# Kernel optimization log

Measured on AMD Instinct MI355X. Metric: run time of the kernel, lower is better.

Reference implementation:

```python
import jax, jax.numpy as jnp
import numpy as np
import math

C_S = 384; C_Z = 128; C_H = 16; H = 12; PQ = 4; PV = 8; C_SURF = 16
N_RES = 512; N_SURF = 2048; B = 1
INF = 1e5; EPS = 1e-8
SOFTPLUS_INV_1 = 0.541324854612918


def _quat_to_rot(q):
    q = q / jnp.linalg.norm(q, axis=-1, keepdims=True)
    w, x, y, z = q[..., 0], q[..., 1], q[..., 2], q[..., 3]
    R = jnp.stack([
        1 - 2 * (y * y + z * z), 2 * (x * y - w * z), 2 * (x * z + w * y),
        2 * (x * y + w * z), 1 - 2 * (x * x + z * z), 2 * (y * z - w * x),
        2 * (x * z - w * y), 2 * (y * z + w * x), 1 - 2 * (x * x + y * y),
    ], axis=-1)
    return R.reshape(q.shape[:-1] + (3, 3))


def setup_inputs() -> dict:
    key = jax.random.key(0)
    ks = jax.random.split(key, 32)
    hc = H * C_H            # 192
    hpq = H * PQ * 3        # 144
    hpkv = H * (PQ + PV) * 3  # 432
    cz4 = C_Z // 4
    concat = hc + H * PV * 3 + H * PV + H * cz4 + hc  # 1152
    w = lambda k, i, o: jax.random.normal(k, (i, o), jnp.float32) * 0.02
    inp = {
        's': jax.random.normal(ks[0], (B, N_RES, C_S), jnp.float32),
        'z': jax.random.normal(ks[1], (B, N_RES, N_RES, C_Z), jnp.float32),
        'rots': _quat_to_rot(jax.random.normal(ks[2], (B, N_RES, 4), jnp.float32)),
        'trans': jax.random.normal(ks[3], (B, N_RES, 3), jnp.float32) * 10.0,
        'mask': jnp.ones((B, N_RES), jnp.float32),
        'surface_points': jax.random.normal(ks[4], (B, N_SURF, 3), jnp.float32) * 10.0,
        'surface_features': jax.random.normal(ks[5], (B, N_SURF, C_SURF), jnp.float32),
        'surface_mask': jnp.ones((B, N_SURF), jnp.float32),
        'Wq': w(ks[6], C_S, hc), 'bq': jnp.zeros((hc,)),
        'Wkv': w(ks[7], C_S, 2 * hc), 'bkv': jnp.zeros((2 * hc,)),
        'Wqp': w(ks[8], C_S, hpq), 'bqp': jnp.zeros((hpq,)),
        'Wkvp': w(ks[9], C_S, hpkv), 'bkvp': jnp.zeros((hpkv,)),
        'Wse': w(ks[10], C_SURF, C_S), 'bse': jnp.zeros((C_S,)),
        'Wsq': w(ks[11], C_S, hc), 'bsq': jnp.zeros((hc,)),
        'Wsk': w(ks[12], C_S, hc), 'bsk': jnp.zeros((hc,)),
        'Wsv': w(ks[13], C_S, hc), 'bsv': jnp.zeros((hc,)),
        'Wb': w(ks[14], C_Z, H), 'bb': jnp.zeros((H,)),
        'Wdz': w(ks[15], C_Z, cz4), 'bdz': jnp.zeros((cz4,)),
        'head_weights': jnp.full((H,), SOFTPLUS_INV_1, jnp.float32),
        'sb_weights': jnp.full((1,), SOFTPLUS_INV_1, jnp.float32),
        'Wout': w(ks[16], concat, C_S), 'bout': jnp.zeros((C_S,)),
        'Wso': w(ks[17], 2 * C_S, C_SURF), 'bso': jnp.zeros((C_SURF,)),
    }
    return inp


def reference(s, z, rots, trans, mask, surface_points, surface_features, surface_mask,
              Wq, bq, Wkv, bkv, Wqp, bqp, Wkvp, bkvp, Wse, bse, Wsq, bsq, Wsk, bsk,
              Wsv, bsv, Wb, bb, Wdz, bdz, head_weights, sb_weights, Wout, bout, Wso, bso):
    lin = lambda x, W, b: x @ W + b
    b_, n, _ = s.shape
    m = surface_points.shape[-2]

    surface_feat = lin(surface_features, Wse, bse)                    # [B,M,c_s]
    # backbone<->surface squared distances
    disp = trans[:, :, None, :] - surface_points[:, None, :, :]       # [B,N,M,3]
    dist_sq = jnp.sum(disp * disp, -1)                                # [B,N,M]

    q = lin(s, Wq, bq).reshape(b_, n, H, C_H)
    kv = lin(s, Wkv, bkv).reshape(b_, n, H, 2 * C_H)
    k, v = kv[..., :C_H], kv[..., C_H:]

    # query points: split into 3 coord chunks, stack, rigid-apply
    qp = lin(s, Wqp, bqp)
    qp = jnp.stack(jnp.split(qp, 3, axis=-1), axis=-1)                # [B,N,H*PQ,3]
    qp = jnp.einsum('bnij,bnpj->bnpi', rots, qp) + trans[:, :, None]
    qp = qp.reshape(b_, n, H, PQ, 3)

    kvp = lin(s, Wkvp, bkvp)
    kvp = jnp.stack(jnp.split(kvp, 3, axis=-1), axis=-1)              # [B,N,H*(PQ+PV),3]
    kvp = jnp.einsum('bnij,bnpj->bnpi', rots, kvp) + trans[:, :, None]
    kvp = kvp.reshape(b_, n, H, PQ + PV, 3)
    kp, vp = kvp[..., :PQ, :], kvp[..., PQ:, :]

    b_bias = lin(z, Wb, bb)                                           # [B,N,N,H]
    a = jnp.einsum('bihc,bjhc->bhij', q, k) * math.sqrt(1.0 / (3 * C_H))
    a = a + math.sqrt(1.0 / 3) * jnp.transpose(b_bias, (0, 3, 1, 2))

    # point-distance attention term
    pt = jnp.sum((qp[:, :, None] - kp[:, None]) ** 2, axis=-1)        # [B,N,N,H,PQ]
    hw = jax.nn.softplus(head_weights)                                # [H]
    pt = jnp.sum(pt, axis=-1) * hw * math.sqrt(1.0 / (3 * (PQ * 9.0 / 2))) * (-0.5)
    a = a + jnp.transpose(pt, (0, 3, 1, 2))                           # [B,H,N,N]

    sq_mask = INF * (mask[:, :, None] * mask[:, None, :] - 1.0)
    a = jax.nn.softmax(a + sq_mask[:, None], axis=-1)

    o = jnp.einsum('bhij,bjhc->bihc', a, v).reshape(b_, n, H * C_H)
    o_pt = jnp.einsum('bhij,bjhpd->bihpd', a, vp)                     # [B,N,H,PV,3]
    o_pt = jnp.einsum('bnji,bnhpj->bnhpi', rots, o_pt - trans[:, :, None, None])
    o_pt_norm = jnp.sqrt(jnp.sum(o_pt ** 2, -1) + EPS).reshape(b_, n, H * PV)
    o_pt_flat = o_pt.reshape(b_, n, H * PV, 3)

    pair_z = lin(z, Wdz, bdz)                                         # [B,N,N,cz/4]
    o_pair = jnp.einsum('bhij,bijc->bihc', a, pair_z).reshape(b_, n, -1)

    # surface cross-attention branch
    sq = lin(s, Wsq, bsq).reshape(b_, n, H, C_H)
    sk = lin(surface_feat, Wsk, bsk).reshape(b_, m, H, C_H)
    sv = lin(surface_feat, Wsv, bsv).reshape(b_, m, H, C_H)
    logits = jnp.einsum('bnhc,bmhc->bhnm', sq, sk) * math.sqrt(1.0 / C_H)
    sbw = jax.nn.softplus(sb_weights)[0]
    logits = logits - 0.5 * sbw * dist_sq[:, None]
    cross_mask = mask[:, :, None] * surface_mask[:, None, :]          # [B,N,M]
    logits = logits + INF * (cross_mask - 1.0)[:, None]
    a_s = jax.nn.softmax(logits, axis=-1)
    o_surf = jnp.einsum('bhnm,bmhc->bnhc', a_s, sv).reshape(b_, n, H * C_H)

    o_cat = jnp.concatenate([o, o_pt_flat[..., 0], o_pt_flat[..., 1], o_pt_flat[..., 2],
                             o_pt_norm, o_pair, o_surf], axis=-1)
    s_out = lin(o_cat, Wout, bout)                                    # [B,N,c_s]

    # surface update: attend surface points to backbone (softmax over residues)
    a_ts = jax.nn.softmax(jnp.swapaxes(logits, -1, -2), axis=-1).mean(axis=1)  # [B,M,N]
    s_agg = jnp.einsum('bmn,bnc->bmc', a_ts, s)
    surf_out = lin(jnp.concatenate([surface_feat, s_agg], axis=-1), Wso, bso)
    return s_out, surf_out
```

## Files before the change

### kernel.cpp

```cpp
#include <hip/hip_runtime.h>
#include <cstddef>


#define CS 384
#define INFV 100000.0f

__device__ __forceinline__ float softplusf(float x) { return log1pf(__expf(x)); }

__global__ __launch_bounds__(256) void k_pack(
    const float* __restrict__ Wq, const float* __restrict__ Wsq,
    const float* __restrict__ Wkv, const float* __restrict__ Wqp,
    const float* __restrict__ Wkvp, const float* __restrict__ Wsk,
    const float* __restrict__ Wsv, const float* __restrict__ Wout,
    const float* __restrict__ bq, const float* __restrict__ bsq,
    const float* __restrict__ bkv, const float* __restrict__ bqp,
    const float* __restrict__ bkvp, const float* __restrict__ bsk,
    const float* __restrict__ bsv,
    float* __restrict__ wt1, float* __restrict__ wt2, float* __restrict__ wt3,
    float* __restrict__ b1, float* __restrict__ b2)
{
    const int b = blockIdx.x, t = threadIdx.x;
    if (b >= 1092) {
        int idx = (b - 1092) * 256 + t;
        if (idx < 1344) {
            float v;
            if (idx < 192) v = bq[idx];
            else if (idx < 384) v = bsq[idx - 192];
            else if (idx < 768) v = bkv[idx - 384];
            else if (idx < 912) v = bqp[idx - 768];
            else v = bkvp[idx - 912];
            b1[idx] = v;
        } else if (idx < 1728) {
            int i2 = idx - 1344;
            b2[i2] = (i2 < 192) ? bsk[i2] : bsv[i2 - 192];
        }
        return;
    }
    const float* src; float* dst; int C, coff, tile, ldd;
    if (b < 72)       { src = Wq;   C = 192; dst = wt1; coff = 0;   ldd = 384;  tile = b; }
    else if (b < 144) { src = Wsq;  C = 192; dst = wt1; coff = 192; ldd = 384;  tile = b - 72; }
    else if (b < 288) { src = Wkv;  C = 384; dst = wt1; coff = 384; ldd = 384;  tile = b - 144; }
    else if (b < 348) { src = Wqp;  C = 144; dst = wt1; coff = 768; ldd = 384;  tile = b - 288; }
    else if (b < 516) { src = Wkvp; C = 432; dst = wt1; coff = 912; ldd = 384;  tile = b - 348; }
    else if (b < 588) { src = Wsk;  C = 192; dst = wt2; coff = 0;   ldd = 384;  tile = b - 516; }
    else if (b < 660) { src = Wsv;  C = 192; dst = wt2; coff = 192; ldd = 384;  tile = b - 588; }
    else              { src = Wout; C = 384; dst = wt3; coff = 0;   ldd = 1152; tile = b - 660; }
    const int cT = (C + 31) >> 5;
    const int tk = tile / cT, tc = tile % cT;
    __shared__ float l[32][33];
    const int tr = t >> 5, tcc = t & 31;
    #pragma unroll
    for (int rr = 0; rr < 4; ++rr) {
        int kloc = tr * 4 + rr;
        int cg = tc * 32 + tcc;
        l[kloc][tcc] = (cg < C) ? src[(size_t)(tk * 32 + kloc) * C + cg] : 0.f;
    }
    __syncthreads();
    #pragma unroll
    for (int rr = 0; rr < 4; ++rr) {
        int cloc = tr * 4 + rr;
        int cg = tc * 32 + cloc;
        if (cg < C) dst[(size_t)(coff + cg) * ldd + tk * 32 + tcc] = l[tcc][cloc];
    }
}

__global__ __launch_bounds__(256) void k_packz(
    const float* __restrict__ Wb, const float* __restrict__ bb,
    const float* __restrict__ Wdz, const float* __restrict__ bdz,
    float* __restrict__ wz, float* __restrict__ bz)
{
    const float s3 = 0.5773502691896258f;
    int idx = blockIdx.x * 256 + threadIdx.x;
    if (idx < 5632) {
        int c = idx >> 7, kk = idx & 127;
        wz[idx] = (c < 12) ? s3 * Wb[kk * 12 + c] : Wdz[kk * 32 + (c - 12)];
    } else if (idx < 5676) {
        int c = idx - 5632;
        bz[c] = (c < 12) ? s3 * bb[c] : bdz[c - 12];
    }
}

__global__ __launch_bounds__(256) void k_transp(
    const float* __restrict__ A, float* __restrict__ At)
{
    __shared__ float tile[32][33];
    const int r0 = blockIdx.y * 32, c0 = blockIdx.x * 32;
    const int tr = threadIdx.x >> 5, tc = threadIdx.x & 31;
    #pragma unroll
    for (int rr = 0; rr < 4; ++rr)
        tile[tr + rr * 8][tc] = A[(size_t)(r0 + tr + rr * 8) * 384 + c0 + tc];
    __syncthreads();
    #pragma unroll
    for (int rr = 0; rr < 4; ++rr)
        At[(size_t)(c0 + tr + rr * 8) * 512 + r0 + tc] = tile[tc][tr + rr * 8];
}

template<int KTOT, bool HB>
__global__ __launch_bounds__(256) void k_gemm(
    const float* __restrict__ A, const float* __restrict__ Wt,
    const float* __restrict__ bias, float* __restrict__ C, int ldc)
{
    __shared__ float As[64][68];
    __shared__ float Ws[64][68];
    const int t = threadIdx.x;
    const int c0 = blockIdx.x * 64, m0 = blockIdx.y * 64;
    const int sr = t >> 4, sk4 = (t & 15) << 2;
    const int wid = t >> 6, lane = t & 63;
    const int wr = (wid >> 1) * 32, wc = (wid & 1) * 32;
    const int lr = lane >> 3, lc = lane & 7;
    float acc[4][4];
    #pragma unroll
    for (int j = 0; j < 4; ++j) {
        float bv = HB ? bias[c0 + wc + lc + 8 * j] : 0.f;
        #pragma unroll
        for (int i = 0; i < 4; ++i) acc[i][j] = bv;
    }
    for (int kc = 0; kc < KTOT; kc += 64) {
        __syncthreads();
        #pragma unroll
        for (int rep = 0; rep < 4; ++rep) {
            int row = sr + rep * 16;
            *(float4*)&As[row][sk4] = *(const float4*)&A[(size_t)(m0 + row) * KTOT + kc + sk4];
            *(float4*)&Ws[row][sk4] = *(const float4*)&Wt[(size_t)(c0 + row) * KTOT + kc + sk4];
        }
        __syncthreads();
        #pragma unroll 4
        for (int k4 = 0; k4 < 16; ++k4) {
            float4 a[4], w[4];
            #pragma unroll
            for (int i = 0; i < 4; ++i) a[i] = *(float4*)&As[wr + lr + 8 * i][k4 * 4];
            #pragma unroll
            for (int j = 0; j < 4; ++j) w[j] = *(float4*)&Ws[wc + lc + 8 * j][k4 * 4];
            #pragma unroll
            for (int i = 0; i < 4; ++i) {
                #pragma unroll
                for (int j = 0; j < 4; ++j) {
                    acc[i][j] = fmaf(a[i].x, w[j].x, acc[i][j]);
                    acc[i][j] = fmaf(a[i].y, w[j].y, acc[i][j]);
                    acc[i][j] = fmaf(a[i].z, w[j].z, acc[i][j]);
                    acc[i][j] = fmaf(a[i].w, w[j].w, acc[i][j]);
                }
            }
        }
    }
    #pragma unroll
    for (int i = 0; i < 4; ++i) {
        #pragma unroll
        for (int j = 0; j < 4; ++j)
            C[(size_t)(m0 + wr + lr + 8 * i) * ldc + c0 + wc + lc + 8 * j] = acc[i][j];
    }
}

__global__ __launch_bounds__(256) void k_scatter(
    const float* __restrict__ proj, const float* __restrict__ rots,
    const float* __restrict__ trans,
    float* __restrict__ qw, float* __restrict__ kw, float* __restrict__ vw,
    float* __restrict__ sqw, float* __restrict__ qpw, float* __restrict__ kpw,
    float* __restrict__ vpw)
{
    __shared__ float p[4][1344];
    const int n0 = blockIdx.x * 4, t = threadIdx.x;
    for (int idx = t; idx < 1344; idx += 256) {
        #pragma unroll
        for (int r = 0; r < 4; ++r) p[r][idx] = proj[(size_t)(n0 + r) * 1344 + idx];
    }
    __syncthreads();
    for (int idx = t; idx < 3072; idx += 256) {
        int r = idx / 768, c = idx % 768;
        int n = n0 + r;
        float v = p[r][c];
        if (c < 192) qw[(size_t)n * 192 + c] = v;
        else if (c < 384) sqw[(size_t)n * 192 + (c - 192)] = v;
        else {
            int cc = c - 384, h = cc >> 5, sub = cc & 31;
            if (sub < 16) kw[(size_t)n * 192 + h * 16 + sub] = v;
            else          vw[(size_t)n * 192 + h * 16 + (sub - 16)] = v;
        }
    }
    for (int idx = t; idx < 2304; idx += 256) {
        int r = idx / 576, rem = idx % 576;
        int n = n0 + r;
        const float* R = &rots[(size_t)n * 9];
        const float* tr = &trans[(size_t)n * 3];
        if (rem < 144) {
            int pp = rem / 3, d = rem % 3;
            float v = fmaf(R[d*3+0], p[r][768 + pp],
                      fmaf(R[d*3+1], p[r][768 + 48 + pp],
                      fmaf(R[d*3+2], p[r][768 + 96 + pp], tr[d])));
            qpw[(size_t)n * 144 + pp * 3 + d] = v;
        } else {
            int rem2 = rem - 144; int pp = rem2 / 3, d = rem2 % 3;
            float v = fmaf(R[d*3+0], p[r][912 + pp],
                      fmaf(R[d*3+1], p[r][912 + 144 + pp],
                      fmaf(R[d*3+2], p[r][912 + 288 + pp], tr[d])));
            int h = pp / 12, ii = pp % 12;
            if (ii < 4) kpw[(size_t)n * 144 + h * 12 + ii * 3 + d] = v;
            else        vpw[(size_t)n * 288 + h * 24 + (ii - 4) * 3 + d] = v;
        }
    }
}

__global__ __launch_bounds__(256) void k_sfeat(
    const float* __restrict__ sf, const float* __restrict__ Wse,
    const float* __restrict__ bse, float* __restrict__ sfeat)
{
    __shared__ float wl[16 * 384];
    __shared__ float sfl[8][16];
    const int m0 = blockIdx.x * 8, t = threadIdx.x;
    for (int idx = t; idx < 6144; idx += 256) wl[idx] = Wse[idx];
    if (t < 128) sfl[t >> 4][t & 15] = sf[(size_t)(m0 + (t >> 4)) * 16 + (t & 15)];
    __syncthreads();
    #pragma unroll
    for (int u = 0; u < 12; ++u) {
        int idx = t + u * 256;
        int r = idx / 384, c = idx % 384;
        float a = bse[c];
        #pragma unroll
        for (int kk = 0; kk < 16; ++kk) a = fmaf(sfl[r][kk], wl[kk * 384 + c], a);
        sfeat[(size_t)(m0 + r) * 384 + c] = a;
    }
}

__global__ __launch_bounds__(256) void k_zpass(
    const float* __restrict__ z, const float* __restrict__ wz,
    const float* __restrict__ bz, float* __restrict__ bpz)
{
    __shared__ float zt[64][132];
    const int i = blockIdx.x, t = threadIdx.x;
    const int jbase = blockIdx.y * 256;
    const int jl = t & 63;
    const int cgs = __builtin_amdgcn_readfirstlane(t >> 6);
    const float* __restrict__ wp = wz + cgs * 11 * 128;
    float bv[11];
    #pragma unroll
    for (int u = 0; u < 11; ++u) bv[u] = bz[cgs * 11 + u];
    for (int ch = 0; ch < 4; ++ch) {
        const int j0 = jbase + ch * 64;
        __syncthreads();
        for (int idx = t; idx < 2048; idx += 256) {
            int r = idx >> 5, c4 = (idx & 31) << 2;
            *(float4*)&zt[r][c4] = *(const float4*)&z[((size_t)i * 512 + j0 + r) * 128 + c4];
        }
        __syncthreads();
        float acc[11];
        #pragma unroll
        for (int u = 0; u < 11; ++u) acc[u] = bv[u];
        #pragma unroll 2
        for (int k4 = 0; k4 < 128; k4 += 4) {
            float4 zv = *(float4*)&zt[jl][k4];
            #pragma unroll
            for (int u = 0; u < 11; ++u) {
                const float* w = wp + u * 128 + k4;
                acc[u] = fmaf(zv.x, w[0],
                         fmaf(zv.y, w[1],
                         fmaf(zv.z, w[2],
                         fmaf(zv.w, w[3], acc[u]))));
            }
        }
        #pragma unroll
        for (int u = 0; u < 11; ++u)
            bpz[((size_t)i * 44 + cgs * 11 + u) * 512 + j0 + jl] = acc[u];
    }
}

__global__ __launch_bounds__(256) void k_attn_a(
    const float* __restrict__ qw, const float* __restrict__ kw,
    const float* __restrict__ qpw, const float* __restrict__ kpw,
    const float* __restrict__ bpz, const float* __restrict__ mask,
    const float* __restrict__ hwp, float* __restrict__ abuf)
{
    __shared__ float pls[4][520];
    __shared__ float qs[64], qps[48], cpt4[4];
    const int i = blockIdx.x, hg = blockIdx.y;
    const int t = threadIdx.x;
    if (t < 64) qs[t] = qw[(size_t)i * 192 + hg * 64 + t];
    if (t < 48) qps[t] = qpw[(size_t)i * 144 + hg * 48 + t];
    if (t < 4) cpt4[t] = -0.5f * 0.13608276348795434f * softplusf(hwp[hg * 4 + t]);
    const float mask_i = mask[i];
    __syncthreads();
    #pragma unroll 2
    for (int it = 0; it < 8; ++it) {
        int idx = t + it * 256;
        int hh = idx >> 9, j = idx & 511;
        int h = hg * 4 + hh;
        float kj[16], kpj[12];
        { const float4* kr = (const float4*)&kw[(size_t)j * 192 + h * 16];
          *(float4*)&kj[0] = kr[0]; *(float4*)&kj[4] = kr[1];
          *(float4*)&kj[8] = kr[2]; *(float4*)&kj[12] = kr[3]; }
        { const float4* kr = (const float4*)&kpw[(size_t)j * 144 + h * 12];
          *(float4*)&kpj[0] = kr[0]; *(float4*)&kpj[4] = kr[1]; *(float4*)&kpj[8] = kr[2]; }
        float qk = 0.f;
        #pragma unroll
        for (int c = 0; c < 16; ++c) qk = fmaf(qs[hh * 16 + c], kj[c], qk);
        float pts = 0.f;
        #pragma unroll
        for (int p = 0; p < 4; ++p) {
            float dx = qps[hh*12+p*3+0] - kpj[p*3+0];
            float dy = qps[hh*12+p*3+1] - kpj[p*3+1];
            float dz = qps[hh*12+p*3+2] - kpj[p*3+2];
            pts += dx*dx + dy*dy + dz*dz;
        }
        float lg = fmaf(0.14433756729740643f, qk, bpz[((size_t)i * 44 + h) * 512 + j]);
        lg = fmaf(cpt4[hh], pts, lg);
        lg += INFV * (mask_i * mask[j] - 1.0f);
        pls[hh][j] = lg;
    }
    __syncthreads();
    const int w = t >> 6, lane = t & 63;
    float v[8];
    #pragma unroll
    for (int k = 0; k < 8; ++k) v[k] = pls[w][lane + k * 64];
    float mx = v[0];
    #pragma unroll
    for (int k = 1; k < 8; ++k) mx = fmaxf(mx, v[k]);
    #pragma unroll
    for (int off = 32; off; off >>= 1) mx = fmaxf(mx, __shfl_xor(mx, off));
    float sm = 0.f;
    #pragma unroll
    for (int k = 0; k < 8; ++k) { v[k] = __expf(v[k] - mx); sm += v[k]; }
    #pragma unroll
    for (int off = 32; off; off >>= 1) sm += __shfl_xor(sm, off);
    const float inv = 1.0f / sm;
    float* dst = abuf + ((size_t)(hg * 4 + w) * 512 + i) * 512;
    #pragma unroll
    for (int k = 0; k < 8; ++k) dst[lane + k * 64] = v[k] * inv;
}

__global__ __launch_bounds__(256) void k_attn_pair(
    const float* __restrict__ abuf, const float* __restrict__ bpz,
    float* __restrict__ ocat)
{
    __shared__ float al[12][512];
    const int i = blockIdx.x, t = threadIdx.x;
    #pragma unroll
    for (int u = 0; u < 12; ++u) {
        al[u][t] = abuf[(size_t)u * 262144 + (size_t)i * 512 + t];
        al[u][t + 256] = abuf[(size_t)u * 262144 + (size_t)i * 512 + t + 256];
    }
    __syncthreads();
    const int c = t & 31;
    const int h1 = t >> 5;
    const bool dual = (t < 128);
    const float* pz = bpz + ((size_t)i * 44 + 12 + c) * 512;
    const float* a1 = al[h1];
    const float* a2 = al[dual ? h1 + 8 : 0];
    float acc1 = 0.f, acc2 = 0.f;
    for (int j = 0; j < 512; j += 4) {
        float4 p = *(const float4*)&pz[j];
        acc1 = fmaf(a1[j+0], p.x, acc1);
        acc1 = fmaf(a1[j+1], p.y, acc1);
        acc1 = fmaf(a1[j+2], p.z, acc1);
        acc1 = fmaf(a1[j+3], p.w, acc1);
        if (dual) {
            acc2 = fmaf(a2[j+0], p.x, acc2);
            acc2 = fmaf(a2[j+1], p.y, acc2);
            acc2 = fmaf(a2[j+2], p.z, acc2);
            acc2 = fmaf(a2[j+3], p.w, acc2);
        }
    }
    ocat[(size_t)i * 1152 + 576 + h1 * 32 + c] = acc1;
    if (dual) ocat[(size_t)i * 1152 + 576 + (h1 + 8) * 32 + c] = acc2;
}

__global__ __launch_bounds__(256) void k_gemm_ov(
    const float* __restrict__ abuf, const float* __restrict__ vw,
    const float* __restrict__ vpw, float* __restrict__ cbuf)
{
    __shared__ float As[64][68];
    __shared__ float Bs[64][44];
    const int i0 = blockIdx.x * 64, h = blockIdx.y;
    const int t = threadIdx.x;
    const int sr = t >> 4, sk4 = (t & 15) << 2;
    const int r1 = t >> 3;
    const int cb = t & 7;
    float acc[2][5];
    #pragma unroll
    for (int u = 0; u < 5; ++u) { acc[0][u] = 0.f; acc[1][u] = 0.f; }
    for (int kc = 0; kc < 512; kc += 64) {
        __syncthreads();
        #pragma unroll
        for (int rep = 0; rep < 4; ++rep) {
            int row = sr + rep * 16;
            *(float4*)&As[row][sk4] =
                *(const float4*)&abuf[(size_t)h * 262144 + (size_t)(i0 + row) * 512 + kc + sk4];
        }
        #pragma unroll
        for (int u = 0; u < 10; ++u) {
            int idx = t + u * 256;
            int r = idx / 40, cc = idx % 40;
            Bs[r][cc] = (cc < 16) ? vw[(size_t)(kc + r) * 192 + h * 16 + cc]
                                  : vpw[(size_t)(kc + r) * 288 + h * 24 + (cc - 16)];
        }
        __syncthreads();
        #pragma unroll 4
        for (int kk = 0; kk < 64; ++kk) {
            float av1 = As[r1][kk], av2 = As[r1 + 32][kk];
            #pragma unroll
            for (int u = 0; u < 5; ++u) {
                float b = Bs[kk][cb + 8 * u];
                acc[0][u] = fmaf(av1, b, acc[0][u]);
                acc[1][u] = fmaf(av2, b, acc[1][u]);
            }
        }
    }
    #pragma unroll
    for (int u = 0; u < 5; ++u) {
        cbuf[((size_t)h * 512 + i0 + r1) * 40 + cb + 8 * u] = acc[0][u];
        cbuf[((size_t)h * 512 + i0 + r1 + 32) * 40 + cb + 8 * u] = acc[1][u];
    }
}

__global__ __launch_bounds__(256) void k_optfin(
    const float* __restrict__ cbuf, const float* __restrict__ rots,
    const float* __restrict__ trans, float* __restrict__ ocat)
{
    __shared__ float cl[4][12][40];
    const int i0 = blockIdx.x * 4, t = threadIdx.x;
    for (int idx = t; idx < 1920; idx += 256) {
        int ii = idx / 480, rem = idx % 480;
        int h = rem / 40, c = rem % 40;
        cl[ii][h][c] = cbuf[((size_t)h * 512 + i0 + ii) * 40 + c];
    }
    __syncthreads();
    for (int idx = t; idx < 768; idx += 256) {
        int ii = idx / 192, o = idx % 192;
        ocat[(size_t)(i0 + ii) * 1152 + o] = cl[ii][o >> 4][o & 15];
    }
    for (int idx = t; idx < 384; idx += 256) {
        int ii = idx / 96, hp = idx % 96;
        int h = hp >> 3, p = hp & 7;
        int i = i0 + ii;
        const float* R = &rots[(size_t)i * 9];
        float gx = cl[ii][h][16 + p*3 + 0] - trans[(size_t)i*3 + 0];
        float gy = cl[ii][h][16 + p*3 + 1] - trans[(size_t)i*3 + 1];
        float gz = cl[ii][h][16 + p*3 + 2] - trans[(size_t)i*3 + 2];
        float lx = R[0]*gx + R[3]*gy + R[6]*gz;
        float ly = R[1]*gx + R[4]*gy + R[7]*gz;
        float lz = R[2]*gx + R[5]*gy + R[8]*gz;
        float nm = sqrtf(lx*lx + ly*ly + lz*lz + 1e-8f);
        int col = h * 8 + p;
        size_t base = (size_t)i * 1152;
        ocat[base + 192 + col] = lx;
        ocat[base + 288 + col] = ly;
        ocat[base + 384 + col] = lz;
        ocat[base + 480 + col] = nm;
    }
}

__global__ __launch_bounds__(256) void k_surf(
    const float* __restrict__ sqw, const float* __restrict__ skv,
    const float* __restrict__ trans, const float* __restrict__ mask,
    const float* __restrict__ sp, const float* __restrict__ smask,
    const float* __restrict__ sbwp, float* __restrict__ ocat)
{
    __shared__ float sk_t[256][17];
    __shared__ float sv_t[256][17];
    __shared__ float sp_t[768];
    __shared__ float smask_t[256];
    const int h = blockIdx.x >> 5;
    const int n0 = (blockIdx.x & 31) * 16;
    const int t = threadIdx.x;
    const int tn = t >> 4, tm = t & 15;
    const int n = n0 + tn;
    const float sbw = softplusf(sbwp[0]);
    float qreg[16];
    #pragma unroll
    for (int c = 0; c < 16; ++c) qreg[c] = sqw[(size_t)n * 192 + h * 16 + c];
    const float trx = trans[(size_t)n*3+0], tryy = trans[(size_t)n*3+1], trz = trans[(size_t)n*3+2];
    const float mask_n = mask[n];
    float mx = -1e30f, l = 0.f;
    float acc[16];
    #pragma unroll
    for (int c = 0; c < 16; ++c) acc[c] = 0.f;
    for (int tile = 0; tile < 8; ++tile) {
        __syncthreads();
        const int mb = tile * 256;
        for (int idx = t; idx < 1024; idx += 256) {
            int ml = idx >> 2, c4 = (idx & 3) << 2;
            float4 v4 = *(const float4*)&skv[(size_t)(mb + ml) * 384 + h * 16 + c4];
            sk_t[ml][c4+0]=v4.x; sk_t[ml][c4+1]=v4.y; sk_t[ml][c4+2]=v4.z; sk_t[ml][c4+3]=v4.w;
            float4 w4 = *(const float4*)&skv[(size_t)(mb + ml) * 384 + 192 + h * 16 + c4];
            sv_t[ml][c4+0]=w4.x; sv_t[ml][c4+1]=w4.y; sv_t[ml][c4+2]=w4.z; sv_t[ml][c4+3]=w4.w;
        }
        for (int idx = t; idx < 768; idx += 256) sp_t[idx] = sp[(size_t)mb * 3 + idx];
        smask_t[t] = smask[mb + t];
        __syncthreads();
        float lgr[16];
        float tmax = -1e30f;
        #pragma unroll
        for (int kk = 0; kk < 16; ++kk) {
            int ml = tm + (kk << 4);
            float dot = 0.f;
            #pragma unroll
            for (int c = 0; c < 16; ++c) dot = fmaf(qreg[c], sk_t[ml][c], dot);
            float dx = trx - sp_t[ml*3+0], dy = tryy - sp_t[ml*3+1], dz = trz - sp_t[ml*3+2];
            float lg = fmaf(0.25f, dot, -0.5f * sbw * (dx*dx + dy*dy + dz*dz));
            lg += INFV * (mask_n * smask_t[ml] - 1.0f);
            lgr[kk] = lg;
            tmax = fmaxf(tmax, lg);
        }
        float mn = fmaxf(mx, tmax);
        float scale = __expf(mx - mn);
        l *= scale;
        #pragma unroll
        for (int c = 0; c < 16; ++c) acc[c] *= scale;
        #pragma unroll
        for (int kk = 0; kk < 16; ++kk) {
            int ml = tm + (kk << 4);
            float w = __expf(lgr[kk] - mn);
            l += w;
            #pragma unroll
            for (int c = 0; c < 16; ++c) acc[c] = fmaf(w, sv_t[ml][c], acc[c]);
        }
        mx = mn;
    }
    #pragma unroll
    for (int off = 1; off < 16; off <<= 1) {
        float m2 = __shfl_xor(mx, off), l2 = __shfl_xor(l, off);
        float mn = fmaxf(mx, m2);
        float e1 = __expf(mx - mn), e2 = __expf(m2 - mn);
        l = l * e1 + l2 * e2;
        #pragma unroll
        for (int c = 0; c < 16; ++c) {
            float a2 = __shfl_xor(acc[c], off);
            acc[c] = acc[c] * e1 + a2 * e2;
        }
        mx = mn;
    }
    const float invl = 1.0f / l;
    float outv = 0.f;
    #pragma unroll
    for (int c = 0; c < 16; ++c) if (tm == c) outv = acc[c];
    ocat[(size_t)n * 1152 + 960 + h * 16 + tm] = outv * invl;
}

__global__ __launch_bounds__(256) void k_tlog(
    const float* __restrict__ sqw, const float* __restrict__ skv,
    const float* __restrict__ trans, const float* __restrict__ mask,
    const float* __restrict__ sp, const float* __restrict__ smask,
    const float* __restrict__ sbwp, float* __restrict__ logits,
    float* __restrict__ stat_m, float* __restrict__ stat_il)
{
    __shared__ float sk_s[32][16];
    __shared__ float sq_s[32][16];
    __shared__ float trans_s[96];
    __shared__ float mask_s[32];
    __shared__ float spm_s[96];
    __shared__ float smask_s[32];
    const int h = blockIdx.y;
    const int m0 = blockIdx.x * 32;
    const int t = threadIdx.x;
    const int tmg = t >> 5, tnl = t & 31;
    const float sbw = softplusf(sbwp[0]);
    for (int idx = t; idx < 512; idx += 256) {
        int row = idx >> 4, c = idx & 15;
        sk_s[row][c] = skv[(size_t)(m0 + row) * 384 + h * 16 + c];
    }
    if (t < 96) spm_s[t] = sp[(size_t)m0 * 3 + t];
    if (t < 32) smask_s[t] = smask[m0 + t];
    __syncthreads();
    float skr[4][16];
    float spx[4], spy[4], spz[4], smk[4];
    #pragma unroll
    for (int mi = 0; mi < 4; ++mi) {
        int row = tmg * 4 + mi;
        #pragma unroll
        for (int c4 = 0; c4 < 16; c4 += 4)
            *(float4*)&skr[mi][c4] = *(float4*)&sk_s[row][c4];
        spx[mi] = spm_s[row*3+0]; spy[mi] = spm_s[row*3+1]; spz[mi] = spm_s[row*3+2];
        smk[mi] = smask_s[row];
    }
    float mxr[4], lr[4];
    #pragma unroll
    for (int mi = 0; mi < 4; ++mi) { mxr[mi] = -1e30f; lr[mi] = 0.f; }
    for (int nt = 0; nt < 16; ++nt) {
        __syncthreads();
        const int nb = nt * 32;
        if (t < 128) {
            int nn = t >> 2, c4 = (t & 3) << 2;
            *(float4*)&sq_s[nn][c4] = *(const float4*)&sqw[(size_t)(nb + nn) * 192 + h * 16 + c4];
        }
        if (t < 96) trans_s[t] = trans[(size_t)nb * 3 + t];
        if (t < 32) mask_s[t] = mask[nb + t];
        __syncthreads();
        float q[16];
        #pragma unroll
        for (int c4 = 0; c4 < 16; c4 += 4)
            *(float4*)&q[c4] = *(float4*)&sq_s[tnl][c4];
        const float tx = trans_s[tnl*3+0], ty = trans_s[tnl*3+1], tz = trans_s[tnl*3+2];
        const float mkn = mask_s[tnl];
        #pragma unroll
        for (int mi = 0; mi < 4; ++mi) {
            float dot = 0.f;
            #pragma unroll
            for (int c = 0; c < 16; ++c) dot = fmaf(skr[mi][c], q[c], dot);
            float dx = tx - spx[mi], dy = ty - spy[mi], dz = tz - spz[mi];
            float mterm = INFV * (mkn * smk[mi] - 1.0f) - 0.5f * sbw * (dx*dx + dy*dy + dz*dz);
            float lg = fmaf(0.25f, dot, mterm);
            logits[((size_t)(m0 + tmg * 4 + mi) * 12 + h) * 512 + nb + tnl] = lg;
            float newm = fmaxf(mxr[mi], lg);
            lr[mi] = lr[mi] * __expf(mxr[mi] - newm) + __expf(lg - newm);
            mxr[mi] = newm;
        }
    }
    #pragma unroll
    for (int off = 1; off < 32; off <<= 1) {
        #pragma unroll
        for (int mi = 0; mi < 4; ++mi) {
            float m2 = __shfl_xor(mxr[mi], off), l2 = __shfl_xor(lr[mi], off);
            float newm = fmaxf(mxr[mi], m2);
            lr[mi] = lr[mi] * __expf(mxr[mi] - newm) + l2 * __expf(m2 - newm);
            mxr[mi] = newm;
        }
    }
    if (tnl == 0) {
        #pragma unroll
        for (int mi = 0; mi < 4; ++mi) {
            int m = m0 + tmg * 4 + mi;
            stat_m[(size_t)m * 12 + h] = mxr[mi];
            stat_il[(size_t)m * 12 + h] = 1.0f / lr[mi];
        }
    }
}

__global__ __launch_bounds__(256) void k_tw(
    const float* __restrict__ logits, const float* __restrict__ stat_m,
    const float* __restrict__ stat_il, float* __restrict__ w)
{
    __shared__ float mxs[12], ils[12];
    const int m = blockIdx.x, t = threadIdx.x;
    if (t < 12) { mxs[t] = stat_m[(size_t)m * 12 + t]; ils[t] = stat_il[(size_t)m * 12 + t]; }
    __syncthreads();
    const float* lp = logits + (size_t)m * 12 * 512;
    float a0 = 0.f, a1 = 0.f;
    #pragma unroll
    for (int h = 0; h < 12; ++h) {
        a0 += __expf(lp[h * 512 + t] - mxs[h]) * ils[h];
        a1 += __expf(lp[h * 512 + 256 + t] - mxs[h]) * ils[h];
    }
    w[(size_t)m * 512 + t] = a0 * (1.0f / 12.0f);
    w[(size_t)m * 512 + 256 + t] = a1 * (1.0f / 12.0f);
}

__global__ __launch_bounds__(256) void k_surf_out(
    const float* __restrict__ sfeat, const float* __restrict__ saggw,
    const float* __restrict__ Wso, const float* __restrict__ bso,
    float* __restrict__ out)
{
    __shared__ float wl[12304];
    const int t = threadIdx.x;
    for (int idx = t; idx < 12288; idx += 256) {
        int k = idx >> 4, c = idx & 15;
        wl[(k / 192) * 3076 + (k % 192) * 16 + c] = Wso[idx];
    }
    const int m = blockIdx.x * 64 + (t >> 2);
    const int kq = t & 3;
    const float* src = (kq < 2) ? &sfeat[(size_t)m * 384 + kq * 192]
                                : &saggw[(size_t)m * 384 + (kq - 2) * 192];
    __syncthreads();
    float acc[16];
    #pragma unroll
    for (int c = 0; c < 16; ++c) acc[c] = 0.f;
    const float* wb = &wl[kq * 3076];
    for (int k = 0; k < 192; k += 4) {
        float4 v = *(const float4*)&src[k];
        #pragma unroll
        for (int e = 0; e < 4; ++e) {
            float sv = (&v.x)[e];
            #pragma unroll
            for (int c = 0; c < 16; ++c)
                acc[c] = fmaf(sv, wb[(k + e) * 16 + c], acc[c]);
        }
    }
    #pragma unroll
    for (int c = 0; c < 16; ++c) {
        acc[c] += __shfl_xor(acc[c], 1);
        acc[c] += __shfl_xor(acc[c], 2);
    }
    #pragma unroll
    for (int c = 0; c < 16; ++c) {
        if ((c >> 2) == kq) out[196608 + (size_t)m * 16 + c] = acc[c] + bso[c];
    }
}

extern "C" void kernel_launch(void* const* d_in, const int* in_sizes, int n_in,
                              void* d_out, int out_size, void* d_ws, size_t ws_size,
                              hipStream_t stream)
{
    (void)in_sizes; (void)n_in; (void)out_size; (void)ws_size;
    const float* s     = (const float*)d_in[0];
    const float* z     = (const float*)d_in[1];
    const float* rots  = (const float*)d_in[2];
    const float* trans = (const float*)d_in[3];
    const float* mask  = (const float*)d_in[4];
    const float* sp    = (const float*)d_in[5];
    const float* sf    = (const float*)d_in[6];
    const float* smask = (const float*)d_in[7];
    const float* Wq    = (const float*)d_in[8];  const float* bq   = (const float*)d_in[9];
    const float* Wkv   = (const float*)d_in[10]; const float* bkv  = (const float*)d_in[11];
    const float* Wqp   = (const float*)d_in[12]; const float* bqp  = (const float*)d_in[13];
    const float* Wkvp  = (const float*)d_in[14]; const float* bkvp = (const float*)d_in[15];
    const float* Wse   = (const float*)d_in[16]; const float* bse  = (const float*)d_in[17];
    const float* Wsq   = (const float*)d_in[18]; const float* bsq  = (const float*)d_in[19];
    const float* Wsk   = (const float*)d_in[20]; const float* bsk  = (const float*)d_in[21];
    const float* Wsv   = (const float*)d_in[22]; const float* bsv  = (const float*)d_in[23];
    const float* Wb    = (const float*)d_in[24]; const float* bb   = (const float*)d_in[25];
    const float* Wdz   = (const float*)d_in[26]; const float* bdz  = (const float*)d_in[27];
    const float* hw    = (const float*)d_in[28]; const float* sbw  = (const float*)d_in[29];
    const float* Wout  = (const float*)d_in[30]; const float* bout = (const float*)d_in[31];
    const float* Wso   = (const float*)d_in[32]; const float* bso  = (const float*)d_in[33];
    float* out = (float*)d_out;

    float* qw    = (float*)d_ws;
    float* kw    = qw    + (size_t)512 * 192;
    float* vw    = kw    + (size_t)512 * 192;
    float* sqw   = vw    + (size_t)512 * 192;
    float* qpw   = sqw   + (size_t)512 * 192;
    float* kpw   = qpw   + (size_t)512 * 144;
    float* vpw   = kpw   + (size_t)512 * 144;
    float* sfeat = vpw   + (size_t)512 * 288;
    float* skv   = sfeat + (size_t)2048 * 384;
    float* ocat  = skv   + (size_t)2048 * 384;
    float* sagg  = ocat  + (size_t)512 * 1152;
    float* region = sagg + (size_t)2048 * 384;
    float* proj   = region;
    float* bpz    = region;
    float* logits = region;
    float* wt1   = region + (size_t)2048 * 12 * 512;
    float* wt2   = wt1   + (size_t)1344 * 384;
    float* wt3   = wt2   + (size_t)384 * 384;
    float* b1    = wt3   + (size_t)384 * 1152;
    float* b2    = b1    + 1344;
    float* st    = b2    + 384;
    float* wbuf  = st    + (size_t)384 * 512;
    float* statm = wbuf  + (size_t)2048 * 512;
    float* stati = statm + (size_t)2048 * 12;
    float* abuf  = stati + (size_t)2048 * 12;
    float* cbuf  = abuf  + (size_t)12 * 512 * 512;
    float* wz    = cbuf  + (size_t)12 * 512 * 40;
    float* bz    = wz    + (size_t)44 * 128;

    k_pack<<<dim3(1099), dim3(256), 0, stream>>>(Wq, Wsq, Wkv, Wqp, Wkvp, Wsk, Wsv, Wout,
        bq, bsq, bkv, bqp, bkvp, bsk, bsv, wt1, wt2, wt3, b1, b2);
    k_packz<<<dim3(23), dim3(256), 0, stream>>>(Wb, bb, Wdz, bdz, wz, bz);
    k_transp<<<dim3(12, 16), dim3(256), 0, stream>>>(s, st);
    k_gemm<384, true><<<dim3(21, 8), dim3(256), 0, stream>>>(s, wt1, b1, proj, 1344);
    k_scatter<<<dim3(128), dim3(256), 0, stream>>>(proj, rots, trans,
        qw, kw, vw, sqw, qpw, kpw, vpw);
    k_sfeat<<<dim3(256), dim3(256), 0, stream>>>(sf, Wse, bse, sfeat);
    k_gemm<384, true><<<dim3(6, 32), dim3(256), 0, stream>>>(sfeat, wt2, b2, skv, 384);
    k_zpass<<<dim3(512, 2), dim3(256), 0, stream>>>(z, wz, bz, bpz);
    k_attn_a<<<dim3(512, 3), dim3(256), 0, stream>>>(qw, kw, qpw, kpw, bpz, mask, hw, abuf);
    k_attn_pair<<<dim3(512), dim3(256), 0, stream>>>(abuf, bpz, ocat);
    k_gemm_ov<<<dim3(8, 12), dim3(256), 0, stream>>>(abuf, vw, vpw, cbuf);
    k_optfin<<<dim3(128), dim3(256), 0, stream>>>(cbuf, rots, trans, ocat);
    k_surf<<<dim3(384), dim3(256), 0, stream>>>(sqw, skv, trans, mask, sp, smask,
        sbw, ocat);
    k_tlog<<<dim3(64, 12), dim3(256), 0, stream>>>(sqw, skv, trans, mask, sp, smask,
        sbw, logits, statm, stati);
    k_tw<<<dim3(2048), dim3(256), 0, stream>>>(logits, statm, stati, wbuf);
    k_gemm<512, false><<<dim3(6, 32), dim3(256), 0, stream>>>(wbuf, st, nullptr, sagg, 384);
    k_surf_out<<<dim3(32), dim3(256), 0, stream>>>(sfeat, sagg, Wso, bso, out);
    k_gemm<1152, true><<<dim3(6, 8), dim3(256), 0, stream>>>(ocat, wt3, bout, out, 384);
}
```

Baseline: 554.9 us.

## Reuse stored surface logits for residue-side softmax instead of recomputing in k_surf

Removes the fused flash-style k_surf kernel, which recomputed the residue-to-surface logits. The output is now built from the logits buffer already written by k_tlog, using four kernels: per-chunk row max/sum, a combine step, a split-M weighted sum over the surface values, and a final reduction into ocat. This avoids computing the logits twice. In exchange it rereads the 12x2048x512 logits buffer twice from memory and adds three kernel launches.

After: 524.1 us. 1.06x faster.

```diff
diff --git a/kernel.cpp b/kernel.cpp
--- a/kernel.cpp
+++ b/kernel.cpp
@@ -447,93 +447,6 @@
     }
 }
 
-__global__ __launch_bounds__(256) void k_surf(
-    const float* __restrict__ sqw, const float* __restrict__ skv,
-    const float* __restrict__ trans, const float* __restrict__ mask,
-    const float* __restrict__ sp, const float* __restrict__ smask,
-    const float* __restrict__ sbwp, float* __restrict__ ocat)
-{
-    __shared__ float sk_t[256][17];
-    __shared__ float sv_t[256][17];
-    __shared__ float sp_t[768];
-    __shared__ float smask_t[256];
-    const int h = blockIdx.x >> 5;
-    const int n0 = (blockIdx.x & 31) * 16;
-    const int t = threadIdx.x;
-    const int tn = t >> 4, tm = t & 15;
-    const int n = n0 + tn;
-    const float sbw = softplusf(sbwp[0]);
-    float qreg[16];
-    #pragma unroll
-    for (int c = 0; c < 16; ++c) qreg[c] = sqw[(size_t)n * 192 + h * 16 + c];
-    const float trx = trans[(size_t)n*3+0], tryy = trans[(size_t)n*3+1], trz = trans[(size_t)n*3+2];
-    const float mask_n = mask[n];
-    float mx = -1e30f, l = 0.f;
-    float acc[16];
-    #pragma unroll
-    for (int c = 0; c < 16; ++c) acc[c] = 0.f;
-    for (int tile = 0; tile < 8; ++tile) {
-        __syncthreads();
-        const int mb = tile * 256;
-        for (int idx = t; idx < 1024; idx += 256) {
-            int ml = idx >> 2, c4 = (idx & 3) << 2;
-            float4 v4 = *(const float4*)&skv[(size_t)(mb + ml) * 384 + h * 16 + c4];
-            sk_t[ml][c4+0]=v4.x; sk_t[ml][c4+1]=v4.y; sk_t[ml][c4+2]=v4.z; sk_t[ml][c4+3]=v4.w;
-            float4 w4 = *(const float4*)&skv[(size_t)(mb + ml) * 384 + 192 + h * 16 + c4];
-            sv_t[ml][c4+0]=w4.x; sv_t[ml][c4+1]=w4.y; sv_t[ml][c4+2]=w4.z; sv_t[ml][c4+3]=w4.w;
-        }
-        for (int idx = t; idx < 768; idx += 256) sp_t[idx] = sp[(size_t)mb * 3 + idx];
-        smask_t[t] = smask[mb + t];
-        __syncthreads();
-        float lgr[16];
-        float tmax = -1e30f;
-        #pragma unroll
-        for (int kk = 0; kk < 16; ++kk) {
-            int ml = tm + (kk << 4);
-            float dot = 0.f;
-            #pragma unroll
-            for (int c = 0; c < 16; ++c) dot = fmaf(qreg[c], sk_t[ml][c], dot);
-            float dx = trx - sp_t[ml*3+0], dy = tryy - sp_t[ml*3+1], dz = trz - sp_t[ml*3+2];
-            float lg = fmaf(0.25f, dot, -0.5f * sbw * (dx*dx + dy*dy + dz*dz));
-            lg += INFV * (mask_n * smask_t[ml] - 1.0f);
-            lgr[kk] = lg;
-            tmax = fmaxf(tmax, lg);
-        }
-        float mn = fmaxf(mx, tmax);
-        float scale = __expf(mx - mn);
-        l *= scale;
-        #pragma unroll
-        for (int c = 0; c < 16; ++c) acc[c] *= scale;
-        #pragma unroll
-        for (int kk = 0; kk < 16; ++kk) {
-            int ml = tm + (kk << 4);
-            float w = __expf(lgr[kk] - mn);
-            l += w;
-            #pragma unroll
-            for (int c = 0; c < 16; ++c) acc[c] = fmaf(w, sv_t[ml][c], acc[c]);
-        }
-        mx = mn;
-    }
-    #pragma unroll
-    for (int off = 1; off < 16; off <<= 1) {
-        float m2 = __shfl_xor(mx, off), l2 = __shfl_xor(l, off);
-        float mn = fmaxf(mx, m2);
-        float e1 = __expf(mx - mn), e2 = __expf(m2 - mn);
-        l = l * e1 + l2 * e2;
-        #pragma unroll
-        for (int c = 0; c < 16; ++c) {
-            float a2 = __shfl_xor(acc[c], off);
-            acc[c] = acc[c] * e1 + a2 * e2;
-        }
-        mx = mn;
-    }
-    const float invl = 1.0f / l;
-    float outv = 0.f;
-    #pragma unroll
-    for (int c = 0; c < 16; ++c) if (tm == c) outv = acc[c];
-    ocat[(size_t)n * 1152 + 960 + h * 16 + tm] = outv * invl;
-}
-
 __global__ __launch_bounds__(256) void k_tlog(
     const float* __restrict__ sqw, const float* __restrict__ skv,
     const float* __restrict__ trans, const float* __restrict__ mask,
@@ -621,6 +534,118 @@
             stat_il[(size_t)m * 12 + h] = 1.0f / lr[mi];
         }
     }
+}
+
+__global__ __launch_bounds__(256) void k_rstat(
+    const float* __restrict__ lbuf, float* __restrict__ rspm,
+    float* __restrict__ rsps)
+{
+    __shared__ float smx[4][64], ssm[4][64];
+    const int n0 = blockIdx.x * 64, mc = blockIdx.y, h = blockIdx.z;
+    const int t = threadIdx.x, ln = t & 63, mg = t >> 6;
+    const int mb = mc * 512;
+    const int n = n0 + ln;
+    float mx = -1e30f, sm = 0.f;
+    #pragma unroll 2
+    for (int it = 0; it < 128; ++it) {
+        int m = mb + it * 4 + mg;
+        float lg = lbuf[((size_t)m * 12 + h) * 512 + n];
+        float nm = fmaxf(mx, lg);
+        sm = sm * __expf(mx - nm) + __expf(lg - nm);
+        mx = nm;
+    }
+    smx[mg][ln] = mx; ssm[mg][ln] = sm;
+    __syncthreads();
+    if (t < 64) {
+        float M = smx[0][t], S = ssm[0][t];
+        #pragma unroll
+        for (int g = 1; g < 4; ++g) {
+            float m2 = smx[g][t], s2 = ssm[g][t];
+            float nm = fmaxf(M, m2);
+            S = S * __expf(M - nm) + s2 * __expf(m2 - nm);
+            M = nm;
+        }
+        rspm[((size_t)h * 4 + mc) * 512 + n0 + t] = M;
+        rsps[((size_t)h * 4 + mc) * 512 + n0 + t] = S;
+    }
+}
+
+__global__ __launch_bounds__(256) void k_rcomb(
+    const float* __restrict__ rspm, const float* __restrict__ rsps,
+    float* __restrict__ rmax, float* __restrict__ rinv)
+{
+    int gid = blockIdx.x * 256 + threadIdx.x;
+    if (gid >= 6144) return;
+    int h = gid >> 9, n = gid & 511;
+    float M = -1e30f, S = 0.f;
+    #pragma unroll
+    for (int mc = 0; mc < 4; ++mc) {
+        float m2 = rspm[((size_t)h * 4 + mc) * 512 + n];
+        float s2 = rsps[((size_t)h * 4 + mc) * 512 + n];
+        float nm = fmaxf(M, m2);
+        S = S * __expf(M - nm) + s2 * __expf(m2 - nm);
+        M = nm;
+    }
+    rmax[gid] = M;
+    rinv[gid] = 1.0f / S;
+}
+
+__global__ __launch_bounds__(256) void k_pv(
+    const float* __restrict__ lbuf, const float* __restrict__ skv,
+    const float* __restrict__ rmax, const float* __restrict__ rinv,
+    float* __restrict__ pvp)
+{
+    __shared__ float sv_s[512][17];
+    const int n0 = blockIdx.x * 64, mc = blockIdx.y, h = blockIdx.z;
+    const int t = threadIdx.x, ln = t & 63, mg = t >> 6;
+    const int mb = mc * 512;
+    for (int idx = t; idx < 2048; idx += 256) {
+        int ml = idx >> 2, c4 = (idx & 3) << 2;
+        float4 v4 = *(const float4*)&skv[(size_t)(mb + ml) * 384 + 192 + h * 16 + c4];
+        sv_s[ml][c4+0]=v4.x; sv_s[ml][c4+1]=v4.y; sv_s[ml][c4+2]=v4.z; sv_s[ml][c4+3]=v4.w;
+    }
+    const int n = n0 + ln;
+    const float rm = rmax[h * 512 + n], ri = rinv[h * 512 + n];
+    float acc[16];
+    #pragma unroll
+    for (int c = 0; c < 16; ++c) acc[c] = 0.f;
+    __syncthreads();
+    #pragma unroll 2
+    for (int it = 0; it < 128; ++it) {
+        int ml = it * 4 + mg;
+        float w = __expf(lbuf[((size_t)(mb + ml) * 12 + h) * 512 + n] - rm) * ri;
+        #pragma unroll
+        for (int c = 0; c < 16; ++c) acc[c] = fmaf(w, sv_s[ml][c], acc[c]);
+    }
+    __syncthreads();
+    float* red = &sv_s[0][0];
+    #pragma unroll
+    for (int c = 0; c < 16; ++c) red[(mg * 64 + ln) * 17 + c] = acc[c];
+    __syncthreads();
+    {
+        int nl = t >> 2, c4 = (t & 3) << 2;
+        float4 o;
+        #pragma unroll
+        for (int e = 0; e < 4; ++e) {
+            float s = 0.f;
+            #pragma unroll
+            for (int g = 0; g < 4; ++g) s += red[(g * 64 + nl) * 17 + c4 + e];
+            (&o.x)[e] = s;
+        }
+        *(float4*)&pvp[(((size_t)h * 4 + mc) * 512 + n0 + nl) * 16 + c4] = o;
+    }
+}
+
+__global__ __launch_bounds__(256) void k_pvcomb(
+    const float* __restrict__ pvp, float* __restrict__ ocat)
+{
+    int gid = blockIdx.x * 256 + threadIdx.x;
+    int n = gid / 192, rem = gid % 192;
+    float o = 0.f;
+    #pragma unroll
+    for (int mc = 0; mc < 4; ++mc)
+        o += pvp[(((size_t)(rem >> 4) * 4 + mc) * 512 + n) * 16 + (rem & 15)];
+    ocat[(size_t)n * 1152 + 960 + rem] = o;
 }
 
 __global__ __launch_bounds__(256) void k_tw(
@@ -739,6 +764,11 @@
     float* cbuf  = abuf  + (size_t)12 * 512 * 512;
     float* wz    = cbuf  + (size_t)12 * 512 * 40;
     float* bz    = wz    + (size_t)44 * 128;
+    float* rspm  = bz    + 64;
+    float* rsps  = rspm  + (size_t)12 * 4 * 512;
+    float* rmax  = rsps  + (size_t)12 * 4 * 512;
+    float* rinv  = rmax  + (size_t)12 * 512;
+    float* pvp   = rinv  + (size_t)12 * 512;
 
     k_pack<<<dim3(1099), dim3(256), 0, stream>>>(Wq, Wsq, Wkv, Wqp, Wkvp, Wsk, Wsv, Wout,
         bq, bsq, bkv, bqp, bkvp, bsk, bsv, wt1, wt2, wt3, b1, b2);
@@ -754,10 +784,12 @@
     k_attn_pair<<<dim3(512), dim3(256), 0, stream>>>(abuf, bpz, ocat);
     k_gemm_ov<<<dim3(8, 12), dim3(256), 0, stream>>>(abuf, vw, vpw, cbuf);
     k_optfin<<<dim3(128), dim3(256), 0, stream>>>(cbuf, rots, trans, ocat);
-    k_surf<<<dim3(384), dim3(256), 0, stream>>>(sqw, skv, trans, mask, sp, smask,
-        sbw, ocat);
     k_tlog<<<dim3(64, 12), dim3(256), 0, stream>>>(sqw, skv, trans, mask, sp, smask,
         sbw, logits, statm, stati);
+    k_rstat<<<dim3(8, 4, 12), dim3(256), 0, stream>>>(logits, rspm, rsps);
+    k_rcomb<<<dim3(24), dim3(256), 0, stream>>>(rspm, rsps, rmax, rinv);
+    k_pv<<<dim3(8, 4, 12), dim3(256), 0, stream>>>(logits, skv, rmax, rinv, pvp);
+    k_pvcomb<<<dim3(384), dim3(256), 0, stream>>>(pvp, ocat);
     k_tw<<<dim3(2048), dim3(256), 0, stream>>>(logits, statm, stati, wbuf);
     k_gemm<512, false><<<dim3(6, 32), dim3(256), 0, stream>>>(wbuf, st, nullptr, sagg, 384);
     k_surf_out<<<dim3(32), dim3(256), 0, stream>>>(sfeat, sagg, Wso, bso, out);
```
